# Kernel tuning notes

Hardware: AMD Instinct MI355X
Metric: run time of the kernel (lower is better)

## Reference

```python
import jax, jax.numpy as jnp
import numpy as np
import math

B, N, D, H = 4, 2048, 1024, 16
HD = D // H  # head dim = 64


def setup_inputs() -> dict:
    key = jax.random.key(0)
    ks = jax.random.split(key, 5)
    x = jax.random.normal(ks[0], (B, N, D), dtype=jnp.float32)
    # per-head kqv Linear: weight (3*HD, D), bias (3*HD), stacked over heads
    Wkqv = jax.random.normal(ks[1], (H, 3 * HD, D), dtype=jnp.float32) / math.sqrt(D)
    bkqv = jax.random.normal(ks[2], (H, 3 * HD), dtype=jnp.float32) * 0.02
    # output projection Linear(D, D)
    Wproj = jax.random.normal(ks[3], (D, D), dtype=jnp.float32) / math.sqrt(D)
    bproj = jax.random.normal(ks[4], (D,), dtype=jnp.float32) * 0.02
    return {"x": x, "Wkqv": Wkqv, "bkqv": bkqv, "Wproj": Wproj, "bproj": bproj}


def reference(x, Wkqv, bkqv, Wproj, bproj):
    # per-head linear: y = x @ W.T + b  -> [B, H, N, 3*HD]
    kqv = jnp.einsum('bnd,hed->bhne', x, Wkqv) + bkqv[None, :, None, :]
    k, q, v = jnp.split(kqv, 3, axis=-1)  # each [B, H, N, HD]
    # scores = q @ k^T / sqrt(HD)   (attention_scores(k, q) -> q @ k.T)
    scores = jnp.einsum('bhqd,bhkd->bhqk', q, k) / math.sqrt(HD)
    causal = jnp.tril(jnp.ones((N, N), dtype=bool))
    scores = jnp.where(causal[None, None], scores, -jnp.inf)
    att = jax.nn.softmax(scores, axis=-1)
    out = jnp.einsum('bhqk,bhkd->bhqd', att, v)  # [B, H, N, HD]
    # concat heads: [B, N, H*HD]
    sa = out.transpose(0, 2, 1, 3).reshape(B, N, D)
    # dropout is identity in eval mode; final projection
    return sa @ Wproj.T + bproj
```

## Files before the change

### kernel.cpp

```cpp
#include <hip/hip_runtime.h>
#include <hip/hip_bf16.h>


#define NSEQ 2048
#define NHEAD 16
#define DMODEL 1024
#define SCALE2 0.18033688011112042f

typedef __attribute__((ext_vector_type(8))) short v8s;
typedef __attribute__((ext_vector_type(4))) float v4f;

__device__ __forceinline__ float bf2f(unsigned short u) {
    union { unsigned int i; float f; } v;
    v.i = ((unsigned int)u) << 16;
    return v.f;
}
__device__ __forceinline__ unsigned short f2bf(float f) {
    unsigned int x = __float_as_uint(f);
    return (unsigned short)((x + 0x7fffu + ((x >> 16) & 1u)) >> 16);
}
__device__ __forceinline__ unsigned short f2bf_rh(float f) {
    return (unsigned short)((__float_as_uint(f) + 0x8000u) >> 16);
}
__device__ __forceinline__ float fast_exp2(float x) {
#if __has_builtin(__builtin_amdgcn_exp2f)
    return __builtin_amdgcn_exp2f(x);
#else
    return __expf(x * 0.69314718056f);
#endif
}
__device__ __forceinline__ void gld_lds16(const unsigned short* g, unsigned short* l) {
    __builtin_amdgcn_global_load_lds(
        (const __attribute__((address_space(1))) void*)g,
        (__attribute__((address_space(3))) void*)l, 16, 0, 0);
}

__global__ __launch_bounds__(256) void cvt_bf16(
    const float* __restrict__ x, const float* __restrict__ wk, const float* __restrict__ wp,
    unsigned short* __restrict__ xb, unsigned short* __restrict__ wkb,
    unsigned short* __restrict__ wpb)
{
    const int i = blockIdx.x * 256 + threadIdx.x;
    const float* s; unsigned short* d; int o;
    if (i < 2097152)      { s = x;  d = xb;  o = i; }
    else if (i < 2883584) {
        s = wk; d = wkb;
        const int oi  = i - 2097152;
        const int row = oi >> 8, cq = oi & 255;
        const int h   = row / 192;
        const int rem = row - h * 192;
        const int cls = rem >> 6, e = rem & 63;
        float4 f = ((const float4*)s)[oi];
        ushort4 u;
        u.x = f2bf(f.x); u.y = f2bf(f.y); u.z = f2bf(f.z); u.w = f2bf(f.w);
        ((ushort4*)d)[(((cls << 10) + (h << 6) + e) << 8) + cq] = u;
        return;
    }
    else                  { s = wp; d = wpb; o = i - 2883584; }
    float4 f = ((const float4*)s)[o];
    ushort4 u;
    u.x = f2bf(f.x); u.y = f2bf(f.y); u.z = f2bf(f.z); u.w = f2bf(f.w);
    ((ushort4*)d)[o] = u;
}

template <int EPI>
__global__ __launch_bounds__(512, 2) void gemm_lds(
    const unsigned short* __restrict__ A, const unsigned short* __restrict__ B,
    const float* __restrict__ bias,
    float* __restrict__ Cf,
    unsigned short* __restrict__ Kb, unsigned short* __restrict__ Qb,
    unsigned short* __restrict__ VTb,
    int M, int Nc, int K)
{
    __shared__ __align__(16) unsigned short Al[4][8192];
    __shared__ __align__(16) unsigned short Bl[4][8192];

    const int t = threadIdx.x, wave = t >> 6, lane = t & 63;
    const int wm = wave >> 2, wn = wave & 3;

    const int lin = blockIdx.y * gridDim.x + blockIdx.x;
    const int xcd = lin & 7, pos = lin >> 3;
    const int by  = (xcd << 2) + (pos & 3);
    const int bx  = pos >> 2;
    const int m0 = by * 256, n0 = bx * 256;
    const int quad = lane >> 4, c = lane & 15;

    const int g0 = wave * 2, g1 = wave * 2 + 1;
    const int r15 = lane & 15, kg = (lane >> 4) & 3;
    const unsigned short* sA0 = A + (size_t)(m0 + g0 * 16 + r15) * K + kg * 8;
    const unsigned short* sA1 = A + (size_t)(m0 + g1 * 16 + r15) * K + kg * 8;
    const unsigned short* sB0 = B + (size_t)(n0 + g0 * 16 + r15) * K + kg * 8;
    const unsigned short* sB1 = B + (size_t)(n0 + g1 * 16 + r15) * K + kg * 8;

    v4f acc[8][4];
#pragma unroll
    for (int i = 0; i < 8; ++i)
#pragma unroll
        for (int j = 0; j < 4; ++j) acc[i][j] = (v4f){0.f, 0.f, 0.f, 0.f};

    const int fbase = (quad * 16 + c) * 8;
    const int nt = K >> 5;

    auto stageA = [&](int sl, int tt) {
        const int o = tt << 5;
        unsigned short* la = &Al[sl][0];
        gld_lds16(sA0 + o, la + g0 * 512);
        gld_lds16(sA1 + o, la + g1 * 512);
    };
    auto stageB = [&](int sl, int tt) {
        const int o = tt << 5;
        unsigned short* lb = &Bl[sl][0];
        gld_lds16(sB0 + o, lb + g0 * 512);
        gld_lds16(sB1 + o, lb + g1 * 512);
    };

    stageA(0, 0); stageB(0, 0);
    stageA(1, 1); stageB(1, 1);
    stageA(2, 2); stageB(2, 2);
    asm volatile("s_waitcnt vmcnt(8)" ::: "memory");
    __builtin_amdgcn_s_barrier();

    for (int tt = 0; tt < nt; ++tt) {
        const int sl  = tt & 3;
        const int sl3 = (tt + 3) & 3;
        const bool pf = (tt + 3 < nt);

        v8s bfr[4], af[4];
#pragma unroll
        for (int ns = 0; ns < 4; ++ns)
            bfr[ns] = *(const v8s*)&Bl[sl][(wn * 4 + ns) * 512 + fbase];
#pragma unroll
        for (int ms = 0; ms < 4; ++ms)
            af[ms] = *(const v8s*)&Al[sl][(wm * 8 + ms) * 512 + fbase];
        if (pf) stageA(sl3, tt + 3);
        __builtin_amdgcn_s_barrier();
        asm volatile("s_waitcnt lgkmcnt(0)" ::: "memory");
        __builtin_amdgcn_s_setprio(1);
#pragma unroll
        for (int ms = 0; ms < 4; ++ms)
#pragma unroll
            for (int ns = 0; ns < 4; ++ns)
                acc[ms][ns] = __builtin_amdgcn_mfma_f32_16x16x32_bf16(
                    af[ms], bfr[ns], acc[ms][ns], 0, 0, 0);
        __builtin_amdgcn_s_setprio(0);
        __builtin_amdgcn_s_barrier();

        v8s af2[4];
#pragma unroll
        for (int ms = 0; ms < 4; ++ms)
            af2[ms] = *(const v8s*)&Al[sl][(wm * 8 + 4 + ms) * 512 + fbase];
        if (pf) stageB(sl3, tt + 3);
        __builtin_amdgcn_s_barrier();
        asm volatile("s_waitcnt lgkmcnt(0)" ::: "memory");
        __builtin_amdgcn_s_setprio(1);
#pragma unroll
        for (int ms = 0; ms < 4; ++ms)
#pragma unroll
            for (int ns = 0; ns < 4; ++ns)
                acc[4 + ms][ns] = __builtin_amdgcn_mfma_f32_16x16x32_bf16(
                    af2[ms], bfr[ns], acc[4 + ms][ns], 0, 0, 0);
        __builtin_amdgcn_s_setprio(0);
        if (pf)                   { asm volatile("s_waitcnt vmcnt(8)" ::: "memory"); }
        else if (tt + 2 < nt)     { asm volatile("s_waitcnt vmcnt(4)" ::: "memory"); }
        else                      { asm volatile("s_waitcnt vmcnt(0)" ::: "memory"); }
        __builtin_amdgcn_s_barrier();
    }

#pragma unroll
    for (int ms = 0; ms < 8; ++ms) {
        const int row0 = m0 + wm * 128 + ms * 16 + quad * 4;
#pragma unroll
        for (int ns = 0; ns < 4; ++ns) {
            const int colbase = n0 + wn * 64 + ns * 16;
            float bn, scl = 1.f;
            if (EPI == 2) {
                bn = bias[colbase + c];
            } else {
                const int cls = colbase >> 10;
                const int wi  = colbase & 1023;
                const int h   = wi >> 6, e0 = wi & 63;
                bn = bias[h * 192 + cls * 64 + e0 + c];
                if (cls == 1) scl = SCALE2;
            }
            float v0 = (acc[ms][ns][0] + bn) * scl;
            float v1 = (acc[ms][ns][1] + bn) * scl;
            float v2 = (acc[ms][ns][2] + bn) * scl;
            float v3 = (acc[ms][ns][3] + bn) * scl;
            if (EPI == 2) {
                float* pc = Cf + (size_t)row0 * Nc + colbase + c;
                pc[0] = v0; pc[(size_t)Nc] = v1;
                pc[(size_t)2 * Nc] = v2; pc[(size_t)3 * Nc] = v3;
            } else {
                const int cls = colbase >> 10;
                const int wi  = colbase & 1023;
                const int h   = wi >> 6, e = (wi & 63) + c;
                const int bb  = row0 >> 11, tok0 = row0 & 2047;
                const int bhh = bb * 16 + h;
                if (cls == 2) {
                    ushort4 pk;
                    pk.x = f2bf(v0); pk.y = f2bf(v1); pk.z = f2bf(v2); pk.w = f2bf(v3);
                    *(ushort4*)(VTb + ((size_t)bhh * 64 + e) * 2048 + tok0) = pk;
                } else {
                    unsigned short* dst = (cls == 0) ? Kb : Qb;
                    const size_t base = ((size_t)bhh * 2048 + tok0) * 64 + e;
                    dst[base]       = f2bf(v0);
                    dst[base + 64]  = f2bf(v1);
                    dst[base + 128] = f2bf(v2);
                    dst[base + 192] = f2bf(v3);
                }
            }
        }
    }
}

template <bool A_BF16, int EPI>
__global__ __launch_bounds__(256) void gemm_mfma(
    const void* __restrict__ Av, const float* __restrict__ B,
    const float* __restrict__ bias,
    float* __restrict__ Cf,
    unsigned short* __restrict__ Kb, unsigned short* __restrict__ Qb,
    unsigned short* __restrict__ VTb,
    int M, int Nc, int K)
{
    __shared__ __align__(16) unsigned short Al[512 * 8];
    __shared__ __align__(16) unsigned short Bl[512 * 8];

    const int t = threadIdx.x;
    const int wave = t >> 6, lane = t & 63;
    const int wm = wave >> 1, wn = wave & 1;
    const int m0 = blockIdx.y * 128, n0 = blockIdx.x * 128;
    const int quad = lane >> 4, c = lane & 15;

    const int srow = t >> 1, skh = t & 1;
    const int sslot = (srow >> 4) * 64 + (skh * 2) * 16 + (srow & 15);

    v4f acc[4][4];
#pragma unroll
    for (int i = 0; i < 4; ++i)
#pragma unroll
        for (int j = 0; j < 4; ++j) acc[i][j] = (v4f){0.f, 0.f, 0.f, 0.f};

    const unsigned short* pa_u = (const unsigned short*)Av + (size_t)(m0 + srow) * K + skh * 16;
    const float*          pa_f = (const float*)Av          + (size_t)(m0 + srow) * K + skh * 16;
    const float*          pb   = B                          + (size_t)(n0 + srow) * K + skh * 16;

    const int fbase = (quad * 16 + c) * 8;

    for (int k0 = 0; k0 < K; k0 += 32) {
        unsigned short a16[16], b16[16];
        if (A_BF16) {
            uint4 r0 = *(const uint4*)(pa_u + k0);
            uint4 r1 = *(const uint4*)(pa_u + k0 + 8);
            *(uint4*)&a16[0] = r0; *(uint4*)&a16[8] = r1;
        } else {
            float4 f0 = *(const float4*)(pa_f + k0);
            float4 f1 = *(const float4*)(pa_f + k0 + 4);
            float4 f2 = *(const float4*)(pa_f + k0 + 8);
            float4 f3 = *(const float4*)(pa_f + k0 + 12);
            a16[0] = f2bf_rh(f0.x); a16[1] = f2bf_rh(f0.y); a16[2] = f2bf_rh(f0.z); a16[3] = f2bf_rh(f0.w);
            a16[4] = f2bf_rh(f1.x); a16[5] = f2bf_rh(f1.y); a16[6] = f2bf_rh(f1.z); a16[7] = f2bf_rh(f1.w);
            a16[8] = f2bf_rh(f2.x); a16[9] = f2bf_rh(f2.y); a16[10] = f2bf_rh(f2.z); a16[11] = f2bf_rh(f2.w);
            a16[12] = f2bf_rh(f3.x); a16[13] = f2bf_rh(f3.y); a16[14] = f2bf_rh(f3.z); a16[15] = f2bf_rh(f3.w);
        }
        {
            float4 g0 = *(const float4*)(pb + k0);
            float4 g1 = *(const float4*)(pb + k0 + 4);
            float4 g2 = *(const float4*)(pb + k0 + 8);
            float4 g3 = *(const float4*)(pb + k0 + 12);
            b16[0] = f2bf_rh(g0.x); b16[1] = f2bf_rh(g0.y); b16[2] = f2bf_rh(g0.z); b16[3] = f2bf_rh(g0.w);
            b16[4] = f2bf_rh(g1.x); b16[5] = f2bf_rh(g1.y); b16[6] = f2bf_rh(g1.z); b16[7] = f2bf_rh(g1.w);
            b16[8] = f2bf_rh(g2.x); b16[9] = f2bf_rh(g2.y); b16[10] = f2bf_rh(g2.z); b16[11] = f2bf_rh(g2.w);
            b16[12] = f2bf_rh(g3.x); b16[13] = f2bf_rh(g3.y); b16[14] = f2bf_rh(g3.z); b16[15] = f2bf_rh(g3.w);
        }
        __syncthreads();
        *(uint4*)&Al[sslot * 8]        = *(uint4*)&a16[0];
        *(uint4*)&Al[(sslot + 16) * 8] = *(uint4*)&a16[8];
        *(uint4*)&Bl[sslot * 8]        = *(uint4*)&b16[0];
        *(uint4*)&Bl[(sslot + 16) * 8] = *(uint4*)&b16[8];
        __syncthreads();

        v8s af[4], bf[4];
#pragma unroll
        for (int ms = 0; ms < 4; ++ms)
            af[ms] = *(const v8s*)&Al[(wm * 4 + ms) * 512 + fbase];
#pragma unroll
        for (int ns = 0; ns < 4; ++ns)
            bf[ns] = *(const v8s*)&Bl[(wn * 4 + ns) * 512 + fbase];
#pragma unroll
        for (int ms = 0; ms < 4; ++ms)
#pragma unroll
            for (int ns = 0; ns < 4; ++ns)
                acc[ms][ns] = __builtin_amdgcn_mfma_f32_16x16x32_bf16(
                    af[ms], bf[ns], acc[ms][ns], 0, 0, 0);
    }

#pragma unroll
    for (int ms = 0; ms < 4; ++ms) {
        const int row0 = m0 + wm * 64 + ms * 16 + quad * 4;
#pragma unroll
        for (int ns = 0; ns < 4; ++ns) {
            const int colbase = n0 + wn * 64 + ns * 16;
            float bn = (EPI == 2) ? bias[colbase + c] : bias[colbase + c];
            float v0 = acc[ms][ns][0] + bn;
            float v1 = acc[ms][ns][1] + bn;
            float v2 = acc[ms][ns][2] + bn;
            float v3 = acc[ms][ns][3] + bn;
            if (EPI == 2) {
                float* pc = Cf + (size_t)row0 * Nc + colbase + c;
                pc[0] = v0; pc[(size_t)Nc] = v1;
                pc[(size_t)2 * Nc] = v2; pc[(size_t)3 * Nc] = v3;
            } else {
                const int hh = colbase / 192;
                const int eb = colbase - hh * 192;
                const int bb = row0 >> 11, tok0 = row0 & 2047;
                const int bhh = bb * 16 + hh;
                if (eb >= 128) {
                    ushort4 pk;
                    pk.x = f2bf(v0); pk.y = f2bf(v1); pk.z = f2bf(v2); pk.w = f2bf(v3);
                    *(ushort4*)(VTb + ((size_t)bhh * 64 + (eb - 128) + c) * 2048 + tok0) = pk;
                } else {
                    const bool isq = (eb >= 64);
                    const float s = isq ? SCALE2 : 1.f;
                    unsigned short* dst = isq ? Qb : Kb;
                    const int e = (isq ? eb - 64 : eb) + c;
                    const size_t base = ((size_t)bhh * 2048 + tok0) * 64 + e;
                    dst[base]       = f2bf(v0 * s);
                    dst[base + 64]  = f2bf(v1 * s);
                    dst[base + 128] = f2bf(v2 * s);
                    dst[base + 192] = f2bf(v3 * s);
                }
            }
        }
    }
}

#define ATTS 72

__global__ __launch_bounds__(256, 2) void attn_mfma(
    const unsigned short* __restrict__ Kbuf,
    const unsigned short* __restrict__ Qbuf,
    const unsigned short* __restrict__ VT,
    unsigned short* __restrict__ sa)
{
    __shared__ __align__(16) unsigned short Ps[4][64 * ATTS];
    __shared__ __align__(16) float Mrg[2][64][81];

    const int t = threadIdx.x, w = t >> 6, lane = t & 63;
    const int quad = lane >> 4, c = lane & 15;
    const int bh = blockIdx.x & 63, bq = blockIdx.x >> 6;
    const int b = bh >> 4, hh = bh & 15;
    const size_t gbase = (size_t)bh * (2048 * 64);

    const int rs  = c & 3;
    const int rc0 = (quad ^ rs) * 8, rc1 = 32 + rc0;
    unsigned short* PsW = &Ps[w][0];

    const int qtA = (w == 0) ? bq : (w == 1) ? (15 - bq) : (w == 2) ? (16 + bq) : (31 - bq);
    const int kA1 = (w == 0) ? (bq + 1) : (w == 1) ? (16 - bq) : 17;
    const int qtB = (w == 0) ? (31 - bq) : (16 + bq);
    const int kB1 = (w == 0) ? (32 - bq) : (17 + bq);

    v4f oacc[4][4], lacc[4];
    const short oneb = (short)0x3F80;
    const v8s ones = {oneb, oneb, oneb, oneb, oneb, oneb, oneb, oneb};

    auto run_seg = [&](int qt, int k0, int k1) {
        const int qw = qt * 64;
        v8s qf[4][2];
#pragma unroll
        for (int qs = 0; qs < 4; ++qs) {
            const unsigned short* qp =
                Qbuf + gbase + (size_t)(qw + qs * 16 + c) * 64 + quad * 8;
            qf[qs][0] = *(const v8s*)qp;
            qf[qs][1] = *(const v8s*)(qp + 32);
        }
#pragma unroll
        for (int qs = 0; qs < 4; ++qs) {
            lacc[qs] = (v4f){0.f, 0.f, 0.f, 0.f};
#pragma unroll
            for (int dn = 0; dn < 4; ++dn) oacc[qs][dn] = (v4f){0.f, 0.f, 0.f, 0.f};
        }
        for (int kt = k0; kt < k1; ++kt) {
            const int kbase = kt * 64;
            const bool diag = (kt == qt);

            v8s vf[4][2];
#pragma unroll
            for (int dn = 0; dn < 4; ++dn) {
                const unsigned short* vp =
                    VT + gbase + (size_t)(dn * 16 + c) * 2048 + kbase + quad * 8;
                vf[dn][0] = *(const v8s*)vp;
                vf[dn][1] = *(const v8s*)(vp + 32);
            }

#pragma unroll
            for (int kn = 0; kn < 4; ++kn) {
                const unsigned short* kp =
                    Kbuf + gbase + (size_t)(kbase + kn * 16 + c) * 64 + quad * 8;
                v8s kf0 = *(const v8s*)kp;
                v8s kf1 = *(const v8s*)(kp + 32);
#pragma unroll
                for (int qs = 0; qs < 4; ++qs) {
                    v4f s = (v4f){0.f, 0.f, 0.f, 0.f};
                    s = __builtin_amdgcn_mfma_f32_16x16x32_bf16(qf[qs][0], kf0, s, 0, 0, 0);
                    s = __builtin_amdgcn_mfma_f32_16x16x32_bf16(qf[qs][1], kf1, s, 0, 0, 0);
                    if (diag) {
#pragma unroll
                        for (int r = 0; r < 4; ++r)
                            if (kn * 16 + c > qs * 16 + quad * 4 + r) s[r] = -1e30f;
                    }
#pragma unroll
                    for (int r = 0; r < 4; ++r) {
                        const float p = fast_exp2(s[r]);
                        PsW[(qs * 16 + quad * 4 + r) * ATTS +
                            (((2 * kn + (c >> 3)) ^ r) * 8) + (c & 7)] = f2bf_rh(p);
                    }
                }
            }
            v8s pa[4][2];
#pragma unroll
            for (int qs = 0; qs < 4; ++qs) {
                pa[qs][0] = *(const v8s*)&PsW[(qs * 16 + c) * ATTS + rc0];
                pa[qs][1] = *(const v8s*)&PsW[(qs * 16 + c) * ATTS + rc1];
            }
#pragma unroll
            for (int dn = 0; dn < 4; ++dn) {
#pragma unroll
                for (int qs = 0; qs < 4; ++qs) {
                    oacc[qs][dn] = __builtin_amdgcn_mfma_f32_16x16x32_bf16(pa[qs][0], vf[dn][0], oacc[qs][dn], 0, 0, 0);
                    oacc[qs][dn] = __builtin_amdgcn_mfma_f32_16x16x32_bf16(pa[qs][1], vf[dn][1], oacc[qs][dn], 0, 0, 0);
                }
            }
#pragma unroll
            for (int qs = 0; qs < 4; ++qs) {
                lacc[qs] = __builtin_amdgcn_mfma_f32_16x16x32_bf16(pa[qs][0], ones, lacc[qs], 0, 0, 0);
                lacc[qs] = __builtin_amdgcn_mfma_f32_16x16x32_bf16(pa[qs][1], ones, lacc[qs], 0, 0, 0);
            }
        }
    };

    auto store_final = [&](int qt) {
        const int qw = qt * 64;
#pragma unroll
        for (int qs = 0; qs < 4; ++qs) {
            float inv[4];
#pragma unroll
            for (int r = 0; r < 4; ++r) inv[r] = 1.f / lacc[qs][r];
            const size_t obase =
                ((size_t)(b * 2048 + qw + qs * 16 + quad * 4)) * DMODEL + hh * 64;
#pragma unroll
            for (int dn = 0; dn < 4; ++dn)
#pragma unroll
                for (int r = 0; r < 4; ++r)
                    sa[obase + (size_t)r * DMODEL + dn * 16 + c] = f2bf(oacc[qs][dn][r] * inv[r]);
        }
    };

    run_seg(qtA, 0, kA1);
    if (w < 2) {
        store_final(qtA);
        run_seg(qtB, 17, kB1);
        float* mg = &Mrg[w][lane][0];
#pragma unroll
        for (int qs = 0; qs < 4; ++qs) {
#pragma unroll
            for (int dn = 0; dn < 4; ++dn)
#pragma unroll
                for (int r = 0; r < 4; ++r) mg[qs * 16 + dn * 4 + r] = oacc[qs][dn][r];
#pragma unroll
            for (int r = 0; r < 4; ++r) mg[64 + qs * 4 + r] = lacc[qs][r];
        }
    }
    __syncthreads();
    if (w >= 2) {
        const float* mg = &Mrg[3 - w][lane][0];
#pragma unroll
        for (int qs = 0; qs < 4; ++qs) {
#pragma unroll
            for (int dn = 0; dn < 4; ++dn)
#pragma unroll
                for (int r = 0; r < 4; ++r) oacc[qs][dn][r] += mg[qs * 16 + dn * 4 + r];
#pragma unroll
            for (int r = 0; r < 4; ++r) lacc[qs][r] += mg[64 + qs * 4 + r];
        }
        store_final(qtA);
    }
}

extern "C" void kernel_launch(void* const* d_in, const int* in_sizes, int n_in,
                              void* d_out, int out_size, void* d_ws, size_t ws_size,
                              hipStream_t stream) {
    const float* x     = (const float*)d_in[0];
    const float* Wkqv  = (const float*)d_in[1];
    const float* bkqv  = (const float*)d_in[2];
    const float* Wproj = (const float*)d_in[3];
    const float* bproj = (const float*)d_in[4];
    float* out = (float*)d_out;

    unsigned short* Kb = (unsigned short*)d_ws;
    unsigned short* Qb = Kb + (size_t)8388608;
    unsigned short* VT = Qb + (size_t)8388608;
    unsigned short* sa = VT + (size_t)8388608;

    const bool fast = ws_size >= 75497472ull;
    if (fast) {
        unsigned short* xb  = sa;
        unsigned short* wkb = (unsigned short*)d_ws + (size_t)33554432;
        unsigned short* wpb = wkb + (size_t)3145728;
        cvt_bf16<<<12288, 256, 0, stream>>>(x, Wkqv, Wproj, xb, wkb, wpb);
        gemm_lds<1><<<dim3(12, 32), 512, 0, stream>>>(
            xb, wkb, bkqv, nullptr, Kb, Qb, VT, 8192, 3072, 1024);
        attn_mfma<<<512, 256, 0, stream>>>(Kb, Qb, VT, sa);
        gemm_lds<2><<<dim3(4, 32), 512, 0, stream>>>(
            sa, wpb, bproj, out, nullptr, nullptr, nullptr, 8192, 1024, 1024);
    } else {
        gemm_mfma<false, 1><<<dim3(24, 64), 256, 0, stream>>>(
            x, Wkqv, bkqv, nullptr, Kb, Qb, VT, 8192, 3072, 1024);
        attn_mfma<<<512, 256, 0, stream>>>(Kb, Qb, VT, sa);
        gemm_mfma<true, 2><<<dim3(8, 64), 256, 0, stream>>>(
            sa, Wproj, bproj, out, nullptr, nullptr, nullptr, 8192, 1024, 1024);
    }
}
```

Before: 291.6 us.

## Shrink GEMM tile to 128x256 with 3-stage pipeline and higher occupancy

```diff
diff --git a/kernel.cpp b/kernel.cpp
--- a/kernel.cpp
+++ b/kernel.cpp
@@ -64,7 +64,7 @@
 }
 
 template <int EPI>
-__global__ __launch_bounds__(512, 2) void gemm_lds(
+__global__ __launch_bounds__(512, 4) void gemm_lds(
     const unsigned short* __restrict__ A, const unsigned short* __restrict__ B,
     const float* __restrict__ bias,
     float* __restrict__ Cf,
@@ -72,69 +72,60 @@
     unsigned short* __restrict__ VTb,
     int M, int Nc, int K)
 {
-    __shared__ __align__(16) unsigned short Al[4][8192];
-    __shared__ __align__(16) unsigned short Bl[4][8192];
+    __shared__ __align__(16) unsigned short Al[3][4096];
+    __shared__ __align__(16) unsigned short Bl[3][8192];
 
     const int t = threadIdx.x, wave = t >> 6, lane = t & 63;
     const int wm = wave >> 2, wn = wave & 3;
 
     const int lin = blockIdx.y * gridDim.x + blockIdx.x;
     const int xcd = lin & 7, pos = lin >> 3;
-    const int by  = (xcd << 2) + (pos & 3);
-    const int bx  = pos >> 2;
-    const int m0 = by * 256, n0 = bx * 256;
+    const int by  = (xcd << 3) + (pos & 7);
+    const int bx  = pos >> 3;
+    const int m0 = by * 128, n0 = bx * 256;
     const int quad = lane >> 4, c = lane & 15;
 
+    const int r15 = lane & 15, kg = (lane >> 4) & 3;
     const int g0 = wave * 2, g1 = wave * 2 + 1;
-    const int r15 = lane & 15, kg = (lane >> 4) & 3;
-    const unsigned short* sA0 = A + (size_t)(m0 + g0 * 16 + r15) * K + kg * 8;
-    const unsigned short* sA1 = A + (size_t)(m0 + g1 * 16 + r15) * K + kg * 8;
+    const unsigned short* sA  = A + (size_t)(m0 + wave * 16 + r15) * K + kg * 8;
     const unsigned short* sB0 = B + (size_t)(n0 + g0 * 16 + r15) * K + kg * 8;
     const unsigned short* sB1 = B + (size_t)(n0 + g1 * 16 + r15) * K + kg * 8;
 
-    v4f acc[8][4];
-#pragma unroll
-    for (int i = 0; i < 8; ++i)
+    v4f acc[4][4];
+#pragma unroll
+    for (int i = 0; i < 4; ++i)
 #pragma unroll
         for (int j = 0; j < 4; ++j) acc[i][j] = (v4f){0.f, 0.f, 0.f, 0.f};
 
     const int fbase = (quad * 16 + c) * 8;
     const int nt = K >> 5;
 
-    auto stageA = [&](int sl, int tt) {
+    auto stage = [&](int sl, int tt) {
         const int o = tt << 5;
-        unsigned short* la = &Al[sl][0];
-        gld_lds16(sA0 + o, la + g0 * 512);
-        gld_lds16(sA1 + o, la + g1 * 512);
+        gld_lds16(sA  + o, &Al[sl][wave * 512]);
+        gld_lds16(sB0 + o, &Bl[sl][g0 * 512]);
+        gld_lds16(sB1 + o, &Bl[sl][g1 * 512]);
     };
-    auto stageB = [&](int sl, int tt) {
-        const int o = tt << 5;
-        unsigned short* lb = &Bl[sl][0];
-        gld_lds16(sB0 + o, lb + g0 * 512);
-        gld_lds16(sB1 + o, lb + g1 * 512);
-    };
-
-    stageA(0, 0); stageB(0, 0);
-    stageA(1, 1); stageB(1, 1);
-    stageA(2, 2); stageB(2, 2);
-    asm volatile("s_waitcnt vmcnt(8)" ::: "memory");
+
+    stage(0, 0);
+    stage(1, 1);
+    asm volatile("s_waitcnt vmcnt(3)" ::: "memory");
     __builtin_amdgcn_s_barrier();
 
+    int sl = 0;
     for (int tt = 0; tt < nt; ++tt) {
-        const int sl  = tt & 3;
-        const int sl3 = (tt + 3) & 3;
-        const bool pf = (tt + 3 < nt);
-
-        v8s bfr[4], af[4];
+        const int sl2 = (sl == 0) ? 2 : sl - 1;
+        const bool pf = (tt + 2 < nt);
+
+        v8s af[4], bfr[4];
+#pragma unroll
+        for (int ms = 0; ms < 4; ++ms)
+            af[ms] = *(const v8s*)&Al[sl][(wm * 4 + ms) * 512 + fbase];
 #pragma unroll
         for (int ns = 0; ns < 4; ++ns)
             bfr[ns] = *(const v8s*)&Bl[sl][(wn * 4 + ns) * 512 + fbase];
-#pragma unroll
-        for (int ms = 0; ms < 4; ++ms)
-            af[ms] = *(const v8s*)&Al[sl][(wm * 8 + ms) * 512 + fbase];
-        if (pf) stageA(sl3, tt + 3);
-        __builtin_amdgcn_s_barrier();
-        asm volatile("s_waitcnt lgkmcnt(0)" ::: "memory");
+        if (pf) stage(sl2, tt + 2);
+
         __builtin_amdgcn_s_setprio(1);
 #pragma unroll
         for (int ms = 0; ms < 4; ++ms)
@@ -143,32 +134,16 @@
                 acc[ms][ns] = __builtin_amdgcn_mfma_f32_16x16x32_bf16(
                     af[ms], bfr[ns], acc[ms][ns], 0, 0, 0);
         __builtin_amdgcn_s_setprio(0);
+
+        if (pf) { asm volatile("s_waitcnt vmcnt(3)" ::: "memory"); }
+        else    { asm volatile("s_waitcnt vmcnt(0)" ::: "memory"); }
         __builtin_amdgcn_s_barrier();
-
-        v8s af2[4];
-#pragma unroll
-        for (int ms = 0; ms < 4; ++ms)
-            af2[ms] = *(const v8s*)&Al[sl][(wm * 8 + 4 + ms) * 512 + fbase];
-        if (pf) stageB(sl3, tt + 3);
-        __builtin_amdgcn_s_barrier();
-        asm volatile("s_waitcnt lgkmcnt(0)" ::: "memory");
-        __builtin_amdgcn_s_setprio(1);
-#pragma unroll
-        for (int ms = 0; ms < 4; ++ms)
-#pragma unroll
-            for (int ns = 0; ns < 4; ++ns)
-                acc[4 + ms][ns] = __builtin_amdgcn_mfma_f32_16x16x32_bf16(
-                    af2[ms], bfr[ns], acc[4 + ms][ns], 0, 0, 0);
-        __builtin_amdgcn_s_setprio(0);
-        if (pf)                   { asm volatile("s_waitcnt vmcnt(8)" ::: "memory"); }
-        else if (tt + 2 < nt)     { asm volatile("s_waitcnt vmcnt(4)" ::: "memory"); }
-        else                      { asm volatile("s_waitcnt vmcnt(0)" ::: "memory"); }
-        __builtin_amdgcn_s_barrier();
-    }
-
-#pragma unroll
-    for (int ms = 0; ms < 8; ++ms) {
-        const int row0 = m0 + wm * 128 + ms * 16 + quad * 4;
+        sl = (sl == 2) ? 0 : sl + 1;
+    }
+
+#pragma unroll
+    for (int ms = 0; ms < 4; ++ms) {
+        const int row0 = m0 + wm * 64 + ms * 16 + quad * 4;
 #pragma unroll
         for (int ns = 0; ns < 4; ++ns) {
             const int colbase = n0 + wn * 64 + ns * 16;
@@ -508,10 +483,10 @@
         unsigned short* wkb = (unsigned short*)d_ws + (size_t)33554432;
         unsigned short* wpb = wkb + (size_t)3145728;
         cvt_bf16<<<12288, 256, 0, stream>>>(x, Wkqv, Wproj, xb, wkb, wpb);
-        gemm_lds<1><<<dim3(12, 32), 512, 0, stream>>>(
+        gemm_lds<1><<<dim3(12, 64), 512, 0, stream>>>(
             xb, wkb, bkqv, nullptr, Kb, Qb, VT, 8192, 3072, 1024);
         attn_mfma<<<512, 256, 0, stream>>>(Kb, Qb, VT, sa);
-        gemm_lds<2><<<dim3(4, 32), 512, 0, stream>>>(
+        gemm_lds<2><<<dim3(4, 64), 512, 0, stream>>>(
             sa, wpb, bproj, out, nullptr, nullptr, nullptr, 8192, 1024, 1024);
     } else {
         gemm_mfma<false, 1><<<dim3(24, 64), 256, 0, stream>>>(
```

After: 270.6 us (median of 2 runs). 1.08x faster.
